# Kernel optimization log

Measured on AMD Instinct MI355X. Metric: run time of the kernel, lower is better.

## Reference

```python
import jax, jax.numpy as jnp
import numpy as np

N_TOKENS = 4096
D_IN = 1024
NUM_LATENTS = 32768
K = 64


def setup_inputs() -> dict:
    key = jax.random.key(0)
    k1, k2, k3 = jax.random.split(key, 3)
    x = jax.random.normal(k1, (N_TOKENS, D_IN), dtype=jnp.float32)
    # encoder weight, kaiming-ish scale; W_dec initialized as encoder.weight clone
    W_enc = jax.random.normal(k2, (NUM_LATENTS, D_IN), dtype=jnp.float32) / np.sqrt(D_IN)
    W_dec = W_enc.copy()
    # normalize_decoder: unit-norm decoder rows
    W_dec = W_dec / (jnp.linalg.norm(W_dec, axis=-1, keepdims=True) + 1e-8)
    b_enc = jnp.zeros((NUM_LATENTS,), dtype=jnp.float32)
    b_dec = jnp.zeros((D_IN,), dtype=jnp.float32)
    return {"x": x, "W_enc": W_enc, "b_enc": b_enc, "W_dec": W_dec, "b_dec": b_dec, "k": K}


def reference(x, W_enc, b_enc, W_dec, b_dec, k):
    # --- encode: pre_acts = ReLU(encoder(x - b_dec)) ---
    sae_in = x - b_dec                                   # [N, d]
    pre_acts = sae_in @ W_enc.T + b_enc                  # [N, L]
    acts = jax.nn.relu(pre_acts)
    # --- top-k latent selection ---
    top_acts, top_indices = jax.lax.top_k(acts, k)       # [N, k], [N, k]
    # --- sparse gather-based decode ---
    rows = W_dec[top_indices]                            # [N, k, d] gathered decoder rows
    sae_out = jnp.einsum('nk,nkd->nd', top_acts, rows) + b_dec  # [N, d]
    # --- fraction of variance unexplained ---
    e = sae_out - x
    total_variance = jnp.sum((x - jnp.mean(x, axis=0)) ** 2)
    fvu = jnp.sum(e ** 2) / total_variance
    return sae_out, top_acts, top_indices, fvu
```

## Files before the change

kernel.cpp:

```cpp
#include <hip/hip_runtime.h>
#include <math.h>

#define NT 4096
#define DIN 1024
#define NL 32768
#define KSEL 64
#define CAP 512
#define TAU_SIGMA 2.55f
#define BK 64

typedef __attribute__((ext_vector_type(8))) short short8;
typedef __attribute__((ext_vector_type(4))) float f32x4;
typedef unsigned short u16;

__device__ __forceinline__ u16 f2bf(float f) {
  unsigned u = __float_as_uint(f);
  unsigned r = (u + 0x7FFFu + ((u >> 16) & 1u)) >> 16;
  return (u16)r;
}
__device__ __forceinline__ float bf2f(u16 u) {
  return __uint_as_float(((unsigned)u) << 16);
}

__device__ __forceinline__ void gload_lds16(const void* g, void* l) {
  __builtin_amdgcn_global_load_lds(
      (const __attribute__((address_space(1))) void*)g,
      (__attribute__((address_space(3))) void*)l, 16, 0, 0);
}

__global__ __launch_bounds__(256) void prep_x(const float* __restrict__ x,
                                              const float* __restrict__ b_dec,
                                              u16* __restrict__ xin,
                                              float* __restrict__ tau) {
  int t = blockIdx.x, tid = threadIdx.x;
  const float4* xr = (const float4*)(x + (size_t)t * DIN);
  const float4* bd = (const float4*)b_dec;
  float4 v = xr[tid], b = bd[tid];
  float a0 = v.x - b.x, a1 = v.y - b.y, a2 = v.z - b.z, a3 = v.w - b.w;
  ushort4 o;
  o.x = f2bf(a0); o.y = f2bf(a1); o.z = f2bf(a2); o.w = f2bf(a3);
  ((ushort4*)xin)[(size_t)t * 256 + tid] = o;
  float s = a0 * a0 + a1 * a1 + a2 * a2 + a3 * a3;
#pragma unroll
  for (int d = 32; d; d >>= 1) s += __shfl_down(s, d);
  __shared__ float ws_[4];
  int lane = tid & 63, wave = tid >> 6;
  if (lane == 0) ws_[wave] = s;
  __syncthreads();
  if (tid == 0) {
    float tot = ws_[0] + ws_[1] + ws_[2] + ws_[3];
    tau[t] = TAU_SIGMA * sqrtf(tot) * (1.0f / 32.0f);
  }
}

__global__ __launch_bounds__(256) void prep_w(const float* __restrict__ w,
                                              u16* __restrict__ wb, int n4) {
  int i = blockIdx.x * blockDim.x + threadIdx.x;
  int stride = gridDim.x * blockDim.x;
  const float4* w4 = (const float4*)w;
  ushort4* o4 = (ushort4*)wb;
  for (; i < n4; i += stride) {
    float4 v = w4[i];
    ushort4 o;
    o.x = f2bf(v.x); o.y = f2bf(v.y); o.z = f2bf(v.z); o.w = f2bf(v.w);
    o4[i] = o;
  }
}

__global__ __launch_bounds__(256) void colstats(const float* __restrict__ x,
                                                double* __restrict__ colpart) {
  int b = blockIdx.x, tid = threadIdx.x;
  const float4* x4 = (const float4*)x;
  double S0 = 0, S1 = 0, S2 = 0, S3 = 0, Q0 = 0, Q1 = 0, Q2 = 0, Q3 = 0;
  for (int t = b * 32; t < b * 32 + 32; ++t) {
    float4 v = x4[(size_t)t * 256 + tid];
    S0 += v.x; Q0 += (double)v.x * v.x;
    S1 += v.y; Q1 += (double)v.y * v.y;
    S2 += v.z; Q2 += (double)v.z * v.z;
    S3 += v.w; Q3 += (double)v.w * v.w;
  }
  double* p = colpart + ((size_t)b * 256 + tid) * 8;
  p[0] = S0; p[1] = S1; p[2] = S2; p[3] = S3;
  p[4] = Q0; p[5] = Q1; p[6] = Q2; p[7] = Q3;
}

__global__ __launch_bounds__(256, 4) void gemm_select(
    const u16* __restrict__ xin, const u16* __restrict__ wenc,
    const float* __restrict__ b_enc, const float* __restrict__ tau,
    int* __restrict__ cnt, int* __restrict__ cand, float* __restrict__ cscore) {
  __shared__ __align__(16) u16 As[128 * BK];
  __shared__ __align__(16) u16 Bs[128 * BK];
  int bid = blockIdx.x;
  int o = (bid & 7) * 1024 + (bid >> 3);
  int bm = o & 31;
  int bn = o >> 5;
  int tid = threadIdx.x;
  int lane = tid & 63, wave = tid >> 6;

  f32x4 acc[4][4];
#pragma unroll
  for (int m = 0; m < 4; ++m)
#pragma unroll
    for (int n = 0; n < 4; ++n) acc[m][n] = (f32x4)0.0f;

  const u16* pa = xin + (size_t)bm * 128 * DIN +
                  (size_t)(tid >> 3) * DIN + (((tid & 7) ^ ((tid >> 3) & 7)) * 8);
  const u16* pb = wenc + (size_t)bn * 128 * DIN +
                  (size_t)(tid >> 3) * DIN + (((tid & 7) ^ ((tid >> 3) & 7)) * 8);
  u16* Ad = As + wave * 512;
  u16* Bd = Bs + wave * 512;

  int arow = ((wave >> 1) * 64 + (lane & 15)) * BK;
  int brow = ((wave & 1) * 64 + (lane & 15)) * BK;
  int slot0 = lane >> 4;
  int xm = lane & 7;

  for (int kt = 0; kt < 16; ++kt) {
#pragma unroll
    for (int c = 0; c < 4; ++c) {
      gload_lds16(pa + (size_t)(c * 32) * DIN, Ad + c * 2048);
      gload_lds16(pb + (size_t)(c * 32) * DIN, Bd + c * 2048);
    }
    pa += BK; pb += BK;
    __syncthreads();
#pragma unroll
    for (int kk = 0; kk < 2; ++kk) {
      int so = ((kk * 4 + slot0) ^ xm) << 3;
      short8 a[4], b[4];
#pragma unroll
      for (int m = 0; m < 4; ++m) a[m] = *(const short8*)(As + arow + m * 1024 + so);
#pragma unroll
      for (int n = 0; n < 4; ++n) b[n] = *(const short8*)(Bs + brow + n * 1024 + so);
#pragma unroll
      for (int m = 0; m < 4; ++m)
#pragma unroll
        for (int n = 0; n < 4; ++n)
          acc[m][n] = __builtin_amdgcn_mfma_f32_16x16x32_bf16(a[m], b[n], acc[m][n], 0, 0, 0);
    }
    __syncthreads();
  }

  int tok0 = bm * 128 + (wave >> 1) * 64 + ((lane >> 4) << 2);
  int lat0 = bn * 128 + (wave & 1) * 64 + (lane & 15);
#pragma unroll
  for (int n = 0; n < 4; ++n) {
    int latent = lat0 + n * 16;
    float be = b_enc[latent];
#pragma unroll
    for (int m = 0; m < 4; ++m) {
#pragma unroll
      for (int j = 0; j < 4; ++j) {
        float v = acc[m][n][j] + be;
        int tok = tok0 + m * 16 + j;
        if (v > tau[tok]) {
          int p = atomicAdd(cnt + tok, 1);
          if (p < CAP) {
            cand[(size_t)tok * CAP + p] = latent;
            cscore[(size_t)tok * CAP + p] = v;
          }
        }
      }
    }
  }
}

__global__ __launch_bounds__(512) void rescore(
    const float* __restrict__ x, const float* __restrict__ b_dec,
    const float* __restrict__ W_enc, const float* __restrict__ b_enc,
    const float* __restrict__ tau, const int* __restrict__ cnt,
    const int* __restrict__ cand, const float* __restrict__ cscore,
    float* __restrict__ out) {
  int t = blockIdx.x, tid = threadIdx.x;
  __shared__ float sx[DIN];
  __shared__ float ss[CAP];
  __shared__ int sid[CAP];
  __shared__ float sval[CAP];
  __shared__ int sidx[CAP];
  __shared__ float s64sh;
  __shared__ int scnt;
  int m = cnt[t];
  if (m > CAP) m = CAP;
  for (int i = tid; i < DIN; i += 512) sx[i] = x[(size_t)t * DIN + i] - b_dec[i];
  if (tid == 0) scnt = 0;
  if (tid < m) {
    ss[tid] = cscore[(size_t)t * CAP + tid];
    sid[tid] = cand[(size_t)t * CAP + tid];
  }
  __syncthreads();

  float cutoff = -1e30f;
  if (m > KSEL) {
    if (tid < m) {
      float sv = ss[tid];
      int si_ = sid[tid];
      int r = 0;
      for (int j = 0; j < m; ++j) {
        float vj = ss[j];
        int ij = sid[j];
        if (vj > sv || (vj == sv && ij < si_)) ++r;
      }
      if (r == KSEL - 1) s64sh = sv;
    }
    __syncthreads();
    cutoff = s64sh - 0.02f * tau[t];
  }
  if (tid < m && ss[tid] >= cutoff) {
    int p = atomicAdd(&scnt, 1);
    sidx[p] = sid[tid];
  }
  __syncthreads();
  int sc = scnt;

  if (tid < sc) {
    int idx = sidx[tid];
    const float4* wr4 = (const float4*)(W_enc + (size_t)idx * DIN);
    const float4* sx4 = (const float4*)sx;
    float p0 = 0.f, p1 = 0.f;
#pragma unroll 8
    for (int q = 0; q < 128; ++q) {
      float4 w = wr4[q], a = sx4[q];
      p0 = fmaf(a.x, w.x, p0); p0 = fmaf(a.y, w.y, p0);
      p0 = fmaf(a.z, w.z, p0); p0 = fmaf(a.w, w.w, p0);
    }
#pragma unroll 8
    for (int q = 128; q < 256; ++q) {
      float4 w = wr4[q], a = sx4[q];
      p1 = fmaf(a.x, w.x, p1); p1 = fmaf(a.y, w.y, p1);
      p1 = fmaf(a.z, w.z, p1); p1 = fmaf(a.w, w.w, p1);
    }
    float accv = __fadd_rn(p0, p1);
    float pre = __fadd_rn(accv, b_enc[idx]);
    sval[tid] = pre > 0.f ? pre : 0.f;
  }
  __syncthreads();

  float* ta = out + (size_t)NT * DIN;
  float* ti = ta + (size_t)NT * KSEL;
  if (tid < sc) {
    float myv = sval[tid];
    int myi = sidx[tid];
    int rank = 0;
    for (int j = 0; j < sc; ++j) {
      float vj = sval[j];
      int ij = sidx[j];
      if (vj > myv || (vj == myv && ij < myi)) ++rank;
    }
    if (rank < KSEL) {
      ta[(size_t)t * KSEL + rank] = myv;
      ti[(size_t)t * KSEL + rank] = (float)myi;
    }
  }
  if (tid >= sc && tid < KSEL) {
    ta[(size_t)t * KSEL + tid] = 0.f;
    ti[(size_t)t * KSEL + tid] = (float)tid;
  }
}

__global__ __launch_bounds__(256) void decode_bf(
    const float* __restrict__ x, const u16* __restrict__ wdecb,
    const float* __restrict__ b_dec, float* __restrict__ out,
    double* __restrict__ e2part) {
  int t = blockIdx.x, tid = threadIdx.x;
  __shared__ float sa[KSEL];
  __shared__ int si[KSEL];
  __shared__ double sred[4];
  const float* ta = out + (size_t)NT * DIN;
  const float* ti = ta + (size_t)NT * KSEL;
  if (tid < KSEL) {
    sa[tid] = ta[(size_t)t * KSEL + tid];
    si[tid] = (int)ti[(size_t)t * KSEL + tid];
  }
  __syncthreads();
  const float4* bd = (const float4*)b_dec;
  float4 o = bd[tid];
#pragma unroll 4
  for (int k = 0; k < KSEL; ++k) {
    float a = sa[k];
    const ushort4* wr = (const ushort4*)(wdecb + (size_t)si[k] * DIN);
    ushort4 w = wr[tid];
    o.x = fmaf(a, bf2f(w.x), o.x); o.y = fmaf(a, bf2f(w.y), o.y);
    o.z = fmaf(a, bf2f(w.z), o.z); o.w = fmaf(a, bf2f(w.w), o.w);
  }
  ((float4*)out)[(size_t)t * 256 + tid] = o;
  const float4* x4 = (const float4*)(x + (size_t)t * DIN);
  float4 xv = x4[tid];
  float ex = o.x - xv.x, ey = o.y - xv.y, ez = o.z - xv.z, ew = o.w - xv.w;
  double e2 = (double)(ex * ex + ey * ey + ez * ez + ew * ew);
#pragma unroll
  for (int d = 32; d; d >>= 1) e2 += __shfl_down(e2, d);
  int lane = tid & 63, wave = tid >> 6;
  if (lane == 0) sred[wave] = e2;
  __syncthreads();
  if (tid == 0) e2part[t] = sred[0] + sred[1] + sred[2] + sred[3];
}

__global__ __launch_bounds__(256) void decode_f32(
    const float* __restrict__ x, const float* __restrict__ W_dec,
    const float* __restrict__ b_dec, float* __restrict__ out,
    double* __restrict__ e2part) {
  int t = blockIdx.x, tid = threadIdx.x;
  __shared__ float sa[KSEL];
  __shared__ int si[KSEL];
  __shared__ double sred[4];
  const float* ta = out + (size_t)NT * DIN;
  const float* ti = ta + (size_t)NT * KSEL;
  if (tid < KSEL) {
    sa[tid] = ta[(size_t)t * KSEL + tid];
    si[tid] = (int)ti[(size_t)t * KSEL + tid];
  }
  __syncthreads();
  const float4* bd = (const float4*)b_dec;
  float4 o = bd[tid];
#pragma unroll 4
  for (int k = 0; k < KSEL; ++k) {
    float a = sa[k];
    const float4* wr = (const float4*)(W_dec + (size_t)si[k] * DIN);
    float4 w = wr[tid];
    o.x += a * w.x; o.y += a * w.y; o.z += a * w.z; o.w += a * w.w;
  }
  ((float4*)out)[(size_t)t * 256 + tid] = o;
  const float4* x4 = (const float4*)(x + (size_t)t * DIN);
  float4 xv = x4[tid];
  float ex = o.x - xv.x, ey = o.y - xv.y, ez = o.z - xv.z, ew = o.w - xv.w;
  double e2 = (double)(ex * ex + ey * ey + ez * ez + ew * ew);
#pragma unroll
  for (int d = 32; d; d >>= 1) e2 += __shfl_down(e2, d);
  int lane = tid & 63, wave = tid >> 6;
  if (lane == 0) sred[wave] = e2;
  __syncthreads();
  if (tid == 0) e2part[t] = sred[0] + sred[1] + sred[2] + sred[3];
}

__global__ __launch_bounds__(256) void finalize(const double* __restrict__ colpart,
                                                const double* __restrict__ e2part,
                                                float* __restrict__ out) {
  int tid = threadIdx.x;
  double S0 = 0, S1 = 0, S2 = 0, S3 = 0, Q0 = 0, Q1 = 0, Q2 = 0, Q3 = 0;
  for (int b = 0; b < 128; ++b) {
    const double* p = colpart + ((size_t)b * 256 + tid) * 8;
    S0 += p[0]; S1 += p[1]; S2 += p[2]; S3 += p[3];
    Q0 += p[4]; Q1 += p[5]; Q2 += p[6]; Q3 += p[7];
  }
  double tv = (Q0 - S0 * S0 / 4096.0) + (Q1 - S1 * S1 / 4096.0) +
              (Q2 - S2 * S2 / 4096.0) + (Q3 - S3 * S3 / 4096.0);
  double e2 = 0;
  for (int i = tid; i < NT; i += 256) e2 += e2part[i];
#pragma unroll
  for (int d = 32; d; d >>= 1) {
    tv += __shfl_down(tv, d);
    e2 += __shfl_down(e2, d);
  }
  __shared__ double stv[4], se2[4];
  int lane = tid & 63, wave = tid >> 6;
  if (lane == 0) { stv[wave] = tv; se2[wave] = e2; }
  __syncthreads();
  if (tid == 0) {
    double TV = stv[0] + stv[1] + stv[2] + stv[3];
    double E2 = se2[0] + se2[1] + se2[2] + se2[3];
    out[(size_t)NT * DIN + 2 * (size_t)NT * KSEL] = (float)(E2 / TV);
  }
}

extern "C" void kernel_launch(void* const* d_in, const int* in_sizes, int n_in,
                              void* d_out, int out_size, void* d_ws, size_t ws_size,
                              hipStream_t stream) {
  const float* x = (const float*)d_in[0];
  const float* W_enc = (const float*)d_in[1];
  const float* b_enc = (const float*)d_in[2];
  const float* W_dec = (const float*)d_in[3];
  const float* b_dec = (const float*)d_in[4];
  float* out = (float*)d_out;

  char* ws = (char*)d_ws;
  size_t off = 0;
  auto alloc = [&](size_t bytes) -> void* {
    void* p = ws + off;
    off += (bytes + 255) & ~(size_t)255;
    return p;
  };
  double* colpart = (double*)alloc((size_t)128 * 256 * 8 * 8);
  double* e2part = (double*)alloc((size_t)NT * 8);
  float* tau = (float*)alloc((size_t)NT * 4);
  int* cnt = (int*)alloc((size_t)NT * 4);
  int* cand = (int*)alloc((size_t)NT * CAP * 4);
  float* cscore = (float*)alloc((size_t)NT * CAP * 4);
  u16* xin = (u16*)alloc((size_t)NT * DIN * 2);
  u16* wenc = (u16*)alloc((size_t)NL * DIN * 2);
  size_t need_wdec = off + (size_t)NL * DIN * 2;
  u16* wdecb = (ws_size >= need_wdec) ? (u16*)alloc((size_t)NL * DIN * 2) : nullptr;
  (void)in_sizes; (void)n_in; (void)out_size;

  hipMemsetAsync(cnt, 0, (size_t)NT * 4, stream);
  prep_x<<<NT, 256, 0, stream>>>(x, b_dec, xin, tau);
  prep_w<<<2048, 256, 0, stream>>>(W_enc, wenc, NL * DIN / 4);
  if (wdecb) prep_w<<<2048, 256, 0, stream>>>(W_dec, wdecb, NL * DIN / 4);
  colstats<<<128, 256, 0, stream>>>(x, colpart);
  gemm_select<<<(NT / 128) * (NL / 128), 256, 0, stream>>>(xin, wenc, b_enc, tau, cnt, cand, cscore);
  rescore<<<NT, 512, 0, stream>>>(x, b_dec, W_enc, b_enc, tau, cnt, cand, cscore, out);
  if (wdecb)
    decode_bf<<<NT, 256, 0, stream>>>(x, wdecb, b_dec, out, e2part);
  else
    decode_f32<<<NT, 256, 0, stream>>>(x, W_dec, b_dec, out, e2part);
  finalize<<<1, 256, 0, stream>>>(colpart, e2part, out);
}
```

Baseline: 836.8 us.

## Fuse decode into rescore kernel and merge weight conversion launches

Merges the two bf16 weight-conversion launches into one kernel that converts W_enc and W_dec in the same grid-stride loop. Folds the sparse decode and error reduction into the rescore kernel, keeping the top-64 values and indices in shared memory instead of re-reading them from global memory in a separate launch. The rescore dot products are also split across thread pairs, each handling half the row, so more threads share the per-candidate work. This removes kernel launches and global round trips. In exchange the fused kernel uses more shared memory and only half its threads do the decode, which may lower occupancy.

```diff
diff --git a/kernel.cpp b/kernel.cpp
--- a/kernel.cpp
+++ b/kernel.cpp
@@ -53,17 +53,27 @@
   }
 }
 
-__global__ __launch_bounds__(256) void prep_w(const float* __restrict__ w,
-                                              u16* __restrict__ wb, int n4) {
+__global__ __launch_bounds__(256) void prep_w2(const float* __restrict__ w1,
+                                               u16* __restrict__ o1,
+                                               const float* __restrict__ w2,
+                                               u16* __restrict__ o2, int n4) {
   int i = blockIdx.x * blockDim.x + threadIdx.x;
   int stride = gridDim.x * blockDim.x;
-  const float4* w4 = (const float4*)w;
-  ushort4* o4 = (ushort4*)wb;
+  const float4* a4 = (const float4*)w1;
+  const float4* b4 = (const float4*)w2;
+  ushort4* p4 = (ushort4*)o1;
+  ushort4* q4 = (ushort4*)o2;
   for (; i < n4; i += stride) {
-    float4 v = w4[i];
+    float4 v = a4[i];
     ushort4 o;
     o.x = f2bf(v.x); o.y = f2bf(v.y); o.z = f2bf(v.z); o.w = f2bf(v.w);
-    o4[i] = o;
+    p4[i] = o;
+    if (q4) {
+      float4 u = b4[i];
+      ushort4 w;
+      w.x = f2bf(u.x); w.y = f2bf(u.y); w.z = f2bf(u.z); w.w = f2bf(u.w);
+      q4[i] = w;
+    }
   }
 }
 
@@ -164,7 +174,134 @@
   }
 }
 
-__global__ __launch_bounds__(512) void rescore(
+__global__ __launch_bounds__(512) void rescore_fused(
+    const float* __restrict__ x, const float* __restrict__ b_dec,
+    const float* __restrict__ W_enc, const float* __restrict__ b_enc,
+    const float* __restrict__ tau, const int* __restrict__ cnt,
+    const int* __restrict__ cand, const float* __restrict__ cscore,
+    const u16* __restrict__ wdecb, float* __restrict__ out,
+    double* __restrict__ e2part) {
+  int t = blockIdx.x, tid = threadIdx.x;
+  __shared__ float sx[DIN];
+  __shared__ float ss[CAP];
+  __shared__ int sid[CAP];
+  __shared__ float sval[CAP];
+  __shared__ int sidx[CAP];
+  __shared__ float pp[2 * CAP];
+  __shared__ float o64v[KSEL];
+  __shared__ int o64i[KSEL];
+  __shared__ float s64sh;
+  __shared__ int scnt;
+  __shared__ double sred[4];
+  int m = cnt[t];
+  if (m > CAP) m = CAP;
+  for (int i = tid; i < DIN; i += 512) sx[i] = x[(size_t)t * DIN + i] - b_dec[i];
+  if (tid == 0) scnt = 0;
+  if (tid < m) {
+    ss[tid] = cscore[(size_t)t * CAP + tid];
+    sid[tid] = cand[(size_t)t * CAP + tid];
+  }
+  __syncthreads();
+
+  float cutoff = -1e30f;
+  if (m > KSEL) {
+    if (tid < m) {
+      float sv = ss[tid];
+      int si_ = sid[tid];
+      int r = 0;
+      for (int j = 0; j < m; ++j) {
+        float vj = ss[j];
+        int ij = sid[j];
+        if (vj > sv || (vj == sv && ij < si_)) ++r;
+      }
+      if (r == KSEL - 1) s64sh = sv;
+    }
+    __syncthreads();
+    cutoff = s64sh - 0.02f * tau[t];
+  }
+  if (tid < m && ss[tid] >= cutoff) {
+    int p = atomicAdd(&scnt, 1);
+    sidx[p] = sid[tid];
+  }
+  __syncthreads();
+  int sc = scnt;
+
+  {
+    int half = tid & 1;
+    int qb = half * 128;
+    for (int ci = tid >> 1; ci < sc; ci += 256) {
+      int idx = sidx[ci];
+      const float4* wr4 = (const float4*)(W_enc + (size_t)idx * DIN);
+      const float4* sx4 = (const float4*)sx;
+      float p = 0.f;
+#pragma unroll 8
+      for (int q = qb; q < qb + 128; ++q) {
+        float4 w = wr4[q], a = sx4[q];
+        p = fmaf(a.x, w.x, p); p = fmaf(a.y, w.y, p);
+        p = fmaf(a.z, w.z, p); p = fmaf(a.w, w.w, p);
+      }
+      pp[2 * ci + half] = p;
+    }
+  }
+  __syncthreads();
+  for (int ci = tid; ci < sc; ci += 512) {
+    float accv = __fadd_rn(pp[2 * ci], pp[2 * ci + 1]);
+    float pre = __fadd_rn(accv, b_enc[sidx[ci]]);
+    sval[ci] = pre > 0.f ? pre : 0.f;
+  }
+  __syncthreads();
+
+  float* ta = out + (size_t)NT * DIN;
+  float* ti = ta + (size_t)NT * KSEL;
+  for (int ci = tid; ci < sc; ci += 512) {
+    float myv = sval[ci];
+    int myi = sidx[ci];
+    int rank = 0;
+    for (int j = 0; j < sc; ++j) {
+      float vj = sval[j];
+      int ij = sidx[j];
+      if (vj > myv || (vj == myv && ij < myi)) ++rank;
+    }
+    if (rank < KSEL) {
+      ta[(size_t)t * KSEL + rank] = myv;
+      ti[(size_t)t * KSEL + rank] = (float)myi;
+      o64v[rank] = myv;
+      o64i[rank] = myi;
+    }
+  }
+  if (tid >= sc && tid < KSEL) {
+    ta[(size_t)t * KSEL + tid] = 0.f;
+    ti[(size_t)t * KSEL + tid] = (float)tid;
+    o64v[tid] = 0.f;
+    o64i[tid] = tid;
+  }
+  __syncthreads();
+
+  if (tid < 256) {
+    const float4* bd = (const float4*)b_dec;
+    float4 o = bd[tid];
+#pragma unroll 4
+    for (int k = 0; k < KSEL; ++k) {
+      float a = o64v[k];
+      const ushort4* wr = (const ushort4*)(wdecb + (size_t)o64i[k] * DIN);
+      ushort4 w = wr[tid];
+      o.x = fmaf(a, bf2f(w.x), o.x); o.y = fmaf(a, bf2f(w.y), o.y);
+      o.z = fmaf(a, bf2f(w.z), o.z); o.w = fmaf(a, bf2f(w.w), o.w);
+    }
+    ((float4*)out)[(size_t)t * 256 + tid] = o;
+    float4 xv = ((const float4*)(x + (size_t)t * DIN))[tid];
+    float ex = o.x - xv.x, ey = o.y - xv.y, ez = o.z - xv.z, ew = o.w - xv.w;
+    double e2 = (double)(ex * ex + ey * ey + ez * ez + ew * ew);
+#pragma unroll
+    for (int d = 32; d; d >>= 1) e2 += __shfl_down(e2, d);
+    int lane = tid & 63, wave = tid >> 6;
+    if (lane == 0) sred[wave] = e2;
+  }
+  __syncthreads();
+  if (tid == 0) e2part[t] = sred[0] + sred[1] + sred[2] + sred[3];
+}
+
+__global__ __launch_bounds__(512) void rescore_plain(
     const float* __restrict__ x, const float* __restrict__ b_dec,
     const float* __restrict__ W_enc, const float* __restrict__ b_enc,
     const float* __restrict__ tau, const int* __restrict__ cnt,
@@ -187,7 +324,6 @@
     sid[tid] = cand[(size_t)t * CAP + tid];
   }
   __syncthreads();
-
   float cutoff = -1e30f;
   if (m > KSEL) {
     if (tid < m) {
@@ -210,7 +346,6 @@
   }
   __syncthreads();
   int sc = scnt;
-
   if (tid < sc) {
     int idx = sidx[tid];
     const float4* wr4 = (const float4*)(W_enc + (size_t)idx * DIN);
@@ -233,7 +368,6 @@
     sval[tid] = pre > 0.f ? pre : 0.f;
   }
   __syncthreads();
-
   float* ta = out + (size_t)NT * DIN;
   float* ti = ta + (size_t)NT * KSEL;
   if (tid < sc) {
@@ -254,44 +388,6 @@
     ta[(size_t)t * KSEL + tid] = 0.f;
     ti[(size_t)t * KSEL + tid] = (float)tid;
   }
-}
-
-__global__ __launch_bounds__(256) void decode_bf(
-    const float* __restrict__ x, const u16* __restrict__ wdecb,
-    const float* __restrict__ b_dec, float* __restrict__ out,
-    double* __restrict__ e2part) {
-  int t = blockIdx.x, tid = threadIdx.x;
-  __shared__ float sa[KSEL];
-  __shared__ int si[KSEL];
-  __shared__ double sred[4];
-  const float* ta = out + (size_t)NT * DIN;
-  const float* ti = ta + (size_t)NT * KSEL;
-  if (tid < KSEL) {
-    sa[tid] = ta[(size_t)t * KSEL + tid];
-    si[tid] = (int)ti[(size_t)t * KSEL + tid];
-  }
-  __syncthreads();
-  const float4* bd = (const float4*)b_dec;
-  float4 o = bd[tid];
-#pragma unroll 4
-  for (int k = 0; k < KSEL; ++k) {
-    float a = sa[k];
-    const ushort4* wr = (const ushort4*)(wdecb + (size_t)si[k] * DIN);
-    ushort4 w = wr[tid];
-    o.x = fmaf(a, bf2f(w.x), o.x); o.y = fmaf(a, bf2f(w.y), o.y);
-    o.z = fmaf(a, bf2f(w.z), o.z); o.w = fmaf(a, bf2f(w.w), o.w);
-  }
-  ((float4*)out)[(size_t)t * 256 + tid] = o;
-  const float4* x4 = (const float4*)(x + (size_t)t * DIN);
-  float4 xv = x4[tid];
-  float ex = o.x - xv.x, ey = o.y - xv.y, ez = o.z - xv.z, ew = o.w - xv.w;
-  double e2 = (double)(ex * ex + ey * ey + ez * ez + ew * ew);
-#pragma unroll
-  for (int d = 32; d; d >>= 1) e2 += __shfl_down(e2, d);
-  int lane = tid & 63, wave = tid >> 6;
-  if (lane == 0) sred[wave] = e2;
-  __syncthreads();
-  if (tid == 0) e2part[t] = sred[0] + sred[1] + sred[2] + sred[3];
 }
 
 __global__ __launch_bounds__(256) void decode_f32(
@@ -319,8 +415,7 @@
     o.x += a * w.x; o.y += a * w.y; o.z += a * w.z; o.w += a * w.w;
   }
   ((float4*)out)[(size_t)t * 256 + tid] = o;
-  const float4* x4 = (const float4*)(x + (size_t)t * DIN);
-  float4 xv = x4[tid];
+  float4 xv = ((const float4*)(x + (size_t)t * DIN))[tid];
   float ex = o.x - xv.x, ey = o.y - xv.y, ez = o.z - xv.z, ew = o.w - xv.w;
   double e2 = (double)(ex * ex + ey * ey + ez * ez + ew * ew);
 #pragma unroll
@@ -392,14 +487,16 @@
 
   hipMemsetAsync(cnt, 0, (size_t)NT * 4, stream);
   prep_x<<<NT, 256, 0, stream>>>(x, b_dec, xin, tau);
-  prep_w<<<2048, 256, 0, stream>>>(W_enc, wenc, NL * DIN / 4);
-  if (wdecb) prep_w<<<2048, 256, 0, stream>>>(W_dec, wdecb, NL * DIN / 4);
+  prep_w2<<<2048, 256, 0, stream>>>(W_enc, wenc, W_dec, wdecb, NL * DIN / 4);
   colstats<<<128, 256, 0, stream>>>(x, colpart);
   gemm_select<<<(NT / 128) * (NL / 128), 256, 0, stream>>>(xin, wenc, b_enc, tau, cnt, cand, cscore);
-  rescore<<<NT, 512, 0, stream>>>(x, b_dec, W_enc, b_enc, tau, cnt, cand, cscore, out);
-  if (wdecb)
-    decode_bf<<<NT, 256, 0, stream>>>(x, wdecb, b_dec, out, e2part);
-  else
+  if (wdecb) {
+    rescore_fused<<<NT, 512, 0, stream>>>(x, b_dec, W_enc, b_enc, tau, cnt, cand,
+                                          cscore, wdecb, out, e2part);
+  } else {
+    rescore_plain<<<NT, 512, 0, stream>>>(x, b_dec, W_enc, b_enc, tau, cnt, cand,
+                                          cscore, out);
     decode_f32<<<NT, 256, 0, stream>>>(x, W_dec, b_dec, out, e2part);
+  }
   finalize<<<1, 256, 0, stream>>>(colpart, e2part, out);
 }
```

After: 837.8 us. About the same (+0.1%).
